# Optimization experiments

Hardware: AMD Instinct MI355X
Metric: run time of the kernel (lower is better)

Reference implementation:

```python
import jax, jax.numpy as jnp
import numpy as np

B, N, H, T = 128, 512, 128, 4

def setup_inputs() -> dict:
    key = jax.random.key(0)
    ks = jax.random.split(key, 16)
    stdv = 1.0 / np.sqrt(H)
    u = lambda k, shape: jax.random.uniform(k, shape, jnp.float32, -stdv, stdv)
    return {
        "A": jax.random.uniform(ks[0], (B, N, N), jnp.float32),
        "hidden": jax.random.normal(ks[1], (B, N, H), jnp.float32),
        "b_ah": u(ks[2], (H,)),
        "w_z": u(ks[3], (H, H)), "b_wz": u(ks[4], (H,)),
        "u_z": u(ks[5], (H, H)), "b_uz": u(ks[6], (H,)),
        "w_r": u(ks[7], (H, H)), "b_wr": u(ks[8], (H,)),
        "u_r": u(ks[9], (H, H)), "b_ur": u(ks[10], (H,)),
        "w": u(ks[11], (H, H)), "b_w": u(ks[12], (H,)),
        "u": u(ks[13], (H, H)), "b_u": u(ks[14], (H,)),
    }

def reference(A, hidden, b_ah, w_z, b_wz, u_z, b_uz, w_r, b_wr, u_r, b_ur, w, b_w, u, b_u):
    # A: [B,N,N], hidden: [B,N,H]. F.linear(x, W, b) == x @ W.T + b
    def cell(h, _):
        # a = A^T @ h + b_ah  -> [B,N,H]
        a = jnp.einsum('bmn,bmh->bnh', A, h) + b_ah
        z = jax.nn.sigmoid(a @ w_z.T + b_wz + h @ u_z.T + b_uz)
        r = jax.nn.sigmoid(a @ w_r.T + b_wr + h @ u_r.T + b_ur)
        c = jnp.tanh(a @ w.T + b_w + (r * h) @ u.T + b_u)
        h_t = (1.0 - z) * h + z * c
        return h_t, None
    h_out, _ = jax.lax.scan(cell, hidden, None, length=T)
    return h_out
```

## Files before the change

kernel.cpp:

```cpp
#include <hip/hip_runtime.h>
#include <hip/hip_fp16.h>

#define BB 128
#define NN 512
#define HH 128
#define TT 4

typedef _Float16 f16;
typedef _Float16 half8 __attribute__((ext_vector_type(8)));
typedef float floatx4 __attribute__((ext_vector_type(4)));

__device__ __forceinline__ void split1(float x, f16& hi, f16& lo) {
  hi = (f16)x;
  lo = (f16)(x - (float)hi);
}


__global__ void k_wsplit(const float* __restrict__ wz, const float* __restrict__ uz,
                         const float* __restrict__ wr, const float* __restrict__ ur,
                         const float* __restrict__ wc, const float* __restrict__ uc,
                         f16* __restrict__ whi, f16* __restrict__ wlo) {
  int mat = blockIdx.x >> 6;
  int idx = ((blockIdx.x & 63) << 8) + threadIdx.x;
  const float* src = mat==0?wz : mat==1?uz : mat==2?wr : mat==3?ur : mat==4?wc : uc;
  float v = src[idx] * 16.0f;
  f16 hi, lo; split1(v, hi, lo);
  whi[mat*16384 + idx] = hi;
  wlo[mat*16384 + idx] = lo;
}

__global__ void k_bsum(const float* __restrict__ bwz, const float* __restrict__ buz,
                       const float* __restrict__ bwr, const float* __restrict__ bur,
                       const float* __restrict__ bw,  const float* __restrict__ bu,
                       float* __restrict__ bias3) {
  int b = blockIdx.x, j = threadIdx.x;
  bias3[b*HH + j] = b==0 ? bwz[j]+buz[j] : (b==1 ? bwr[j]+bur[j] : bw[j]+bu[j]);
}

__global__ void k_copy_h0(const float* __restrict__ hin, float* __restrict__ h) {
  int v = blockIdx.x * 256 + threadIdx.x;
  ((float4*)h)[v] = ((const float4*)hin)[v];
}


__global__ __launch_bounds__(256) void k_biggemm(const float* __restrict__ A,
                                                 const float* __restrict__ h,
                                                 const float* __restrict__ b_ah,
                                                 float* __restrict__ a32) {
  __shared__ __align__(16) f16 Ah[128*64], Al[128*64], Hh[128*64], Hl[128*64];
  const int b = blockIdx.y, n0 = blockIdx.x * 128, tid = threadIdx.x;
  const int w = tid >> 6, L = tid & 63, quad = L >> 4, l16 = L & 15;
  const int rowsel = tid >> 5, colsel = tid & 31;
  const float* Ab = A + (size_t)b * NN * NN;
  const float* hb = h + (size_t)b * NN * HH;
  const floatx4 zero = {0.f, 0.f, 0.f, 0.f};
  floatx4 acc[2][8];
  for (int sr = 0; sr < 2; sr++) for (int sc = 0; sc < 8; sc++) acc[sr][sc] = zero;

  for (int mc = 0; mc < NN; mc += 64) {
    float4 va[8], vh[8];
#pragma unroll
    for (int i = 0; i < 8; i++) {
      int mm = rowsel * 8 + i;
      va[i] = *(const float4*)(Ab + (size_t)(mc + mm) * NN + n0 + colsel * 4);
      vh[i] = *(const float4*)(hb + (size_t)(mc + mm) * HH + colsel * 4);
    }
#pragma unroll
    for (int q = 0; q < 4; q++) {
      int c = colsel * 4 + q;
      half8 avh, avl, hvh, hvl;
#pragma unroll
      for (int i = 0; i < 8; i++) {
        f16 hi, lo;
        split1(((const float*)&va[i])[q], hi, lo); avh[i] = hi; avl[i] = lo;
        split1(((const float*)&vh[i])[q], hi, lo); hvh[i] = hi; hvl[i] = lo;
      }
      int blk = (rowsel ^ (c & 7)) * 8;
      *(half8*)&Ah[c*64 + blk] = avh;  *(half8*)&Al[c*64 + blk] = avl;
      *(half8*)&Hh[c*64 + blk] = hvh;  *(half8*)&Hl[c*64 + blk] = hvl;
    }
    __syncthreads();
#pragma unroll
    for (int ks = 0; ks < 2; ks++) {
      const int kb = ks * 4 + quad;
      half8 afh[2], afl[2], bfh[8], bfl[8];
      for (int sr = 0; sr < 2; sr++) {
        int c = w*32 + sr*16 + l16, o = c*64 + ((kb ^ (c & 7)) * 8);
        afh[sr] = *(const half8*)&Ah[o];
        afl[sr] = *(const half8*)&Al[o];
      }
      for (int sc = 0; sc < 8; sc++) {
        int c = sc*16 + l16, o = c*64 + ((kb ^ (c & 7)) * 8);
        bfh[sc] = *(const half8*)&Hh[o];
        bfl[sc] = *(const half8*)&Hl[o];
      }
      for (int sr = 0; sr < 2; sr++)
        for (int sc = 0; sc < 8; sc++) {
          acc[sr][sc] = __builtin_amdgcn_mfma_f32_16x16x32_f16(afh[sr], bfh[sc], acc[sr][sc], 0, 0, 0);
          acc[sr][sc] = __builtin_amdgcn_mfma_f32_16x16x32_f16(afh[sr], bfl[sc], acc[sr][sc], 0, 0, 0);
          acc[sr][sc] = __builtin_amdgcn_mfma_f32_16x16x32_f16(afl[sr], bfh[sc], acc[sr][sc], 0, 0, 0);
        }
    }
    __syncthreads();
  }
  float bah[8];
  for (int sc = 0; sc < 8; sc++) bah[sc] = b_ah[sc*16 + l16];
  float* ab = a32 + (size_t)b * NN * HH;
#pragma unroll
  for (int sr = 0; sr < 2; sr++)
    for (int rg = 0; rg < 4; rg++) {
      const int row = n0 + w*32 + sr*16 + quad*4 + rg;
      for (int sc = 0; sc < 8; sc++)
        ab[(size_t)row*HH + sc*16 + l16] = acc[sr][sc][rg] + bah[sc];
    }
}

__global__ __launch_bounds__(256) void k_gates(const float* __restrict__ a32,
                                               float* __restrict__ h,
                                               const f16* __restrict__ whi,
                                               const f16* __restrict__ wlo,
                                               const float* __restrict__ bias3) {
  __shared__ __align__(16) f16 rhh[128*136], rhl[128*136];
  const int row0 = blockIdx.x << 7, tid = threadIdx.x;
  const int w = tid >> 6, L = tid & 63, quad = L >> 4, l16 = L & 15;
  const float* ap[2]; const float* hp[2];
  for (int sr = 0; sr < 2; sr++) {
    int r = row0 + w*32 + sr*16 + l16;
    ap[sr] = a32 + (size_t)r * HH;
    hp[sr] = h + (size_t)r * HH;
  }
  half8 afh[2][4], afl[2][4];
#pragma unroll
  for (int sr = 0; sr < 2; sr++)
#pragma unroll
    for (int ks = 0; ks < 4; ks++) {
      const int ko = ks*32 + quad*8;
      float4 p = *(const float4*)(ap[sr] + ko);
      float4 q2 = *(const float4*)(ap[sr] + ko + 4);
      const float* v = (const float*)&p;
      const float* v2 = (const float*)&q2;
      for (int i = 0; i < 4; i++) { f16 hi, lo; split1(v[i],  hi, lo); afh[sr][ks][i]   = hi; afl[sr][ks][i]   = lo; }
      for (int i = 0; i < 4; i++) { f16 hi, lo; split1(v2[i], hi, lo); afh[sr][ks][i+4] = hi; afl[sr][ks][i+4] = lo; }
    }
  const floatx4 zero = {0.f, 0.f, 0.f, 0.f};
  const f16* Wz_h = whi;            const f16* Wz_l = wlo;
  const f16* Uz_h = whi + 16384;    const f16* Uz_l = wlo + 16384;
  const f16* Wr_h = whi + 2*16384;  const f16* Wr_l = wlo + 2*16384;
  const f16* Ur_h = whi + 3*16384;  const f16* Ur_l = wlo + 3*16384;
  const f16* Wc_h = whi + 4*16384;  const f16* Wc_l = wlo + 4*16384;
  const f16* Uc_h = whi + 5*16384;  const f16* Uc_l = wlo + 5*16384;

  floatx4 racc[2][8];
  for (int sr = 0; sr < 2; sr++) for (int sc = 0; sc < 8; sc++) racc[sr][sc] = zero;
#pragma unroll
  for (int ks = 0; ks < 4; ks++) {
    const int ko = ks*32 + quad*8;
    half8 hfh[2], hfl[2];
    for (int sr = 0; sr < 2; sr++) {
      float4 p = *(const float4*)(hp[sr] + ko);
      float4 q2 = *(const float4*)(hp[sr] + ko + 4);
      const float* v = (const float*)&p; const float* v2 = (const float*)&q2;
      for (int i = 0; i < 4; i++) { f16 hi, lo; split1(v[i],  hi, lo); hfh[sr][i]   = hi; hfl[sr][i]   = lo; }
      for (int i = 0; i < 4; i++) { f16 hi, lo; split1(v2[i], hi, lo); hfh[sr][i+4] = hi; hfl[sr][i+4] = lo; }
    }
#pragma unroll
    for (int sc = 0; sc < 8; sc++) {
      const int wo = (sc*16 + l16)*HH + ko;
      half8 wh = *(const half8*)(Wr_h + wo), wl = *(const half8*)(Wr_l + wo);
      half8 uh = *(const half8*)(Ur_h + wo), ul = *(const half8*)(Ur_l + wo);
      for (int sr = 0; sr < 2; sr++) {
        racc[sr][sc] = __builtin_amdgcn_mfma_f32_16x16x32_f16(afh[sr][ks], wh, racc[sr][sc], 0, 0, 0);
        racc[sr][sc] = __builtin_amdgcn_mfma_f32_16x16x32_f16(afh[sr][ks], wl, racc[sr][sc], 0, 0, 0);
        racc[sr][sc] = __builtin_amdgcn_mfma_f32_16x16x32_f16(afl[sr][ks], wh, racc[sr][sc], 0, 0, 0);
        racc[sr][sc] = __builtin_amdgcn_mfma_f32_16x16x32_f16(hfh[sr], uh, racc[sr][sc], 0, 0, 0);
        racc[sr][sc] = __builtin_amdgcn_mfma_f32_16x16x32_f16(hfh[sr], ul, racc[sr][sc], 0, 0, 0);
        racc[sr][sc] = __builtin_amdgcn_mfma_f32_16x16x32_f16(hfl[sr], uh, racc[sr][sc], 0, 0, 0);
      }
    }
  }
  {
    float brv[8];
    for (int sc = 0; sc < 8; sc++) brv[sc] = bias3[128 + sc*16 + l16];
#pragma unroll
    for (int sr = 0; sr < 2; sr++)
#pragma unroll
      for (int rg = 0; rg < 4; rg++) {
        const int lrow = w*32 + sr*16 + quad*4 + rg;
        const float* hrow = h + (size_t)(row0 + lrow)*HH;
        for (int sc = 0; sc < 8; sc++) {
          const int col = sc*16 + l16;
          float pr = racc[sr][sc][rg] * 0.0625f + brv[sc];
          float rv = 1.f / (1.f + expf(-pr));
          float rhv = rv * hrow[col];
          f16 hi, lo; split1(rhv, hi, lo);
          rhh[lrow*136 + col] = hi;
          rhl[lrow*136 + col] = lo;
        }
      }
  }
  __syncthreads();
  floatx4 cacc[2][8];
  for (int sr = 0; sr < 2; sr++) for (int sc = 0; sc < 8; sc++) cacc[sr][sc] = zero;
#pragma unroll
  for (int ks = 0; ks < 4; ks++) {
    const int ko = ks*32 + quad*8;
    half8 rfh[2], rfl[2];
    for (int sr = 0; sr < 2; sr++) {
      int o = (w*32 + sr*16 + l16)*136 + ko;
      rfh[sr] = *(const half8*)&rhh[o];
      rfl[sr] = *(const half8*)&rhl[o];
    }
#pragma unroll
    for (int sc = 0; sc < 8; sc++) {
      const int wo = (sc*16 + l16)*HH + ko;
      half8 wh = *(const half8*)(Wc_h + wo), wl = *(const half8*)(Wc_l + wo);
      half8 uh = *(const half8*)(Uc_h + wo), ul = *(const half8*)(Uc_l + wo);
      for (int sr = 0; sr < 2; sr++) {
        cacc[sr][sc] = __builtin_amdgcn_mfma_f32_16x16x32_f16(afh[sr][ks], wh, cacc[sr][sc], 0, 0, 0);
        cacc[sr][sc] = __builtin_amdgcn_mfma_f32_16x16x32_f16(afh[sr][ks], wl, cacc[sr][sc], 0, 0, 0);
        cacc[sr][sc] = __builtin_amdgcn_mfma_f32_16x16x32_f16(afl[sr][ks], wh, cacc[sr][sc], 0, 0, 0);
        cacc[sr][sc] = __builtin_amdgcn_mfma_f32_16x16x32_f16(rfh[sr], uh, cacc[sr][sc], 0, 0, 0);
        cacc[sr][sc] = __builtin_amdgcn_mfma_f32_16x16x32_f16(rfh[sr], ul, cacc[sr][sc], 0, 0, 0);
        cacc[sr][sc] = __builtin_amdgcn_mfma_f32_16x16x32_f16(rfl[sr], uh, cacc[sr][sc], 0, 0, 0);
      }
    }
  }
  floatx4 zacc[2][8];
  for (int sr = 0; sr < 2; sr++) for (int sc = 0; sc < 8; sc++) zacc[sr][sc] = zero;
#pragma unroll
  for (int ks = 0; ks < 4; ks++) {
    const int ko = ks*32 + quad*8;
    half8 hfh[2], hfl[2];
    for (int sr = 0; sr < 2; sr++) {
      float4 p = *(const float4*)(hp[sr] + ko);
      float4 q2 = *(const float4*)(hp[sr] + ko + 4);
      const float* v = (const float*)&p; const float* v2 = (const float*)&q2;
      for (int i = 0; i < 4; i++) { f16 hi, lo; split1(v[i],  hi, lo); hfh[sr][i]   = hi; hfl[sr][i]   = lo; }
      for (int i = 0; i < 4; i++) { f16 hi, lo; split1(v2[i], hi, lo); hfh[sr][i+4] = hi; hfl[sr][i+4] = lo; }
    }
#pragma unroll
    for (int sc = 0; sc < 8; sc++) {
      const int wo = (sc*16 + l16)*HH + ko;
      half8 wh = *(const half8*)(Wz_h + wo), wl = *(const half8*)(Wz_l + wo);
      half8 uh = *(const half8*)(Uz_h + wo), ul = *(const half8*)(Uz_l + wo);
      for (int sr = 0; sr < 2; sr++) {
        zacc[sr][sc] = __builtin_amdgcn_mfma_f32_16x16x32_f16(afh[sr][ks], wh, zacc[sr][sc], 0, 0, 0);
        zacc[sr][sc] = __builtin_amdgcn_mfma_f32_16x16x32_f16(afh[sr][ks], wl, zacc[sr][sc], 0, 0, 0);
        zacc[sr][sc] = __builtin_amdgcn_mfma_f32_16x16x32_f16(afl[sr][ks], wh, zacc[sr][sc], 0, 0, 0);
        zacc[sr][sc] = __builtin_amdgcn_mfma_f32_16x16x32_f16(hfh[sr], uh, zacc[sr][sc], 0, 0, 0);
        zacc[sr][sc] = __builtin_amdgcn_mfma_f32_16x16x32_f16(hfh[sr], ul, zacc[sr][sc], 0, 0, 0);
        zacc[sr][sc] = __builtin_amdgcn_mfma_f32_16x16x32_f16(hfl[sr], uh, zacc[sr][sc], 0, 0, 0);
      }
    }
  }
  float bzv[8], bcv[8];
  for (int sc = 0; sc < 8; sc++) {
    bzv[sc] = bias3[sc*16 + l16];
    bcv[sc] = bias3[256 + sc*16 + l16];
  }
#pragma unroll
  for (int sr = 0; sr < 2; sr++)
#pragma unroll
    for (int rg = 0; rg < 4; rg++) {
      const int lrow = w*32 + sr*16 + quad*4 + rg;
      float* hrow = h + (size_t)(row0 + lrow)*HH;
      for (int sc = 0; sc < 8; sc++) {
        const int col = sc*16 + l16;
        float pz = zacc[sr][sc][rg] * 0.0625f + bzv[sc];
        float zv = 1.f / (1.f + expf(-pz));
        float cv = tanhf(cacc[sr][sc][rg] * 0.0625f + bcv[sc]);
        float hv = hrow[col];
        hrow[col] = hv + zv*(cv - hv);
      }
    }
}

extern "C" void kernel_launch(void* const* d_in, const int* in_sizes, int n_in,
                              void* d_out, int out_size, void* d_ws, size_t ws_size,
                              hipStream_t stream) {
  const float* A      = (const float*)d_in[0];
  const float* hidden = (const float*)d_in[1];
  const float* b_ah   = (const float*)d_in[2];
  const float* w_z = (const float*)d_in[3];  const float* b_wz = (const float*)d_in[4];
  const float* u_z = (const float*)d_in[5];  const float* b_uz = (const float*)d_in[6];
  const float* w_r = (const float*)d_in[7];  const float* b_wr = (const float*)d_in[8];
  const float* u_r = (const float*)d_in[9];  const float* b_ur = (const float*)d_in[10];
  const float* w   = (const float*)d_in[11]; const float* b_w  = (const float*)d_in[12];
  const float* u   = (const float*)d_in[13]; const float* b_u  = (const float*)d_in[14];

  float* h = (float*)d_out;
  char* ws = (char*)d_ws;
  float* a32  = (float*)ws;
  f16*   whi  = (f16*)(ws + 33554432);
  f16*   wlo  = (f16*)(ws + 33751040);
  float* bias3= (float*)(ws + 33947648);

  k_wsplit<<<384, 256, 0, stream>>>(w_z, u_z, w_r, u_r, w, u, whi, wlo);
  k_bsum<<<3, HH, 0, stream>>>(b_wz, b_uz, b_wr, b_ur, b_w, b_u, bias3);
  k_copy_h0<<<8192, 256, 0, stream>>>(hidden, h);

  for (int t = 0; t < TT; t++) {
    k_biggemm<<<dim3(4, BB), 256, 0, stream>>>(A, h, b_ah, a32);
    k_gates<<<512, 256, 0, stream>>>(a32, h, whi, wlo, bias3);
  }
}
```

Before: 1.008 ms.

## Stage gate weights through LDS with global_load_lds and swizzled layouts

The gate kernel now copies each weight K-slice (hi and lo halves) into a small LDS buffer using global_load_lds direct-to-LDS loads, with an XOR swizzle, instead of having every wave load the weights from global memory into registers. The hidden-state hi/lo splits are computed once up front rather than recomputed per gate, the z-gate GEMM is moved ahead of the c-gate, and the r*h scratch buffer uses a swizzled layout in place of padding. Launch bounds now request two blocks per CU. In exchange it adds many __syncthreads and full vmcnt waits per K step with no double buffering, and keeping hfh/hfl live across the kernel increases register pressure.

```diff
diff --git a/kernel.cpp b/kernel.cpp
--- a/kernel.cpp
+++ b/kernel.cpp
@@ -14,6 +14,10 @@
   hi = (f16)x;
   lo = (f16)(x - (float)hi);
 }
+
+#define GLL16(gp, lp) __builtin_amdgcn_global_load_lds( \
+    (const __attribute__((address_space(1))) void*)(const void*)(gp), \
+    (__attribute__((address_space(3))) void*)(void*)(lp), 16, 0, 0)
 
 
 __global__ void k_wsplit(const float* __restrict__ wz, const float* __restrict__ uz,
@@ -115,21 +119,23 @@
     }
 }
 
-__global__ __launch_bounds__(256) void k_gates(const float* __restrict__ a32,
-                                               float* __restrict__ h,
-                                               const f16* __restrict__ whi,
-                                               const f16* __restrict__ wlo,
-                                               const float* __restrict__ bias3) {
-  __shared__ __align__(16) f16 rhh[128*136], rhl[128*136];
+__global__ __launch_bounds__(256, 2) void k_gates(const float* __restrict__ a32,
+                                                  float* __restrict__ h,
+                                                  const f16* __restrict__ whi,
+                                                  const f16* __restrict__ wlo,
+                                                  const float* __restrict__ bias3) {
+  __shared__ __align__(16) f16 wbuf[8192];
+  __shared__ __align__(16) f16 rhh[16384], rhl[16384];
   const int row0 = blockIdx.x << 7, tid = threadIdx.x;
   const int w = tid >> 6, L = tid & 63, quad = L >> 4, l16 = L & 15;
+
   const float* ap[2]; const float* hp[2];
   for (int sr = 0; sr < 2; sr++) {
     int r = row0 + w*32 + sr*16 + l16;
     ap[sr] = a32 + (size_t)r * HH;
     hp[sr] = h + (size_t)r * HH;
   }
-  half8 afh[2][4], afl[2][4];
+  half8 afh[2][4], afl[2][4], hfh[2][4], hfl[2][4];
 #pragma unroll
   for (int sr = 0; sr < 2; sr++)
 #pragma unroll
@@ -141,8 +147,32 @@
       const float* v2 = (const float*)&q2;
       for (int i = 0; i < 4; i++) { f16 hi, lo; split1(v[i],  hi, lo); afh[sr][ks][i]   = hi; afl[sr][ks][i]   = lo; }
       for (int i = 0; i < 4; i++) { f16 hi, lo; split1(v2[i], hi, lo); afh[sr][ks][i+4] = hi; afl[sr][ks][i+4] = lo; }
+      float4 hpv = *(const float4*)(hp[sr] + ko);
+      float4 hqv = *(const float4*)(hp[sr] + ko + 4);
+      const float* hv1 = (const float*)&hpv;
+      const float* hv2 = (const float*)&hqv;
+      for (int i = 0; i < 4; i++) { f16 hi, lo; split1(hv1[i], hi, lo); hfh[sr][ks][i]   = hi; hfl[sr][ks][i]   = lo; }
+      for (int i = 0; i < 4; i++) { f16 hi, lo; split1(hv2[i], hi, lo); hfh[sr][ks][i+4] = hi; hfl[sr][ks][i+4] = lo; }
     }
   const floatx4 zero = {0.f, 0.f, 0.f, 0.f};
+
+  const int rq = L >> 2;
+  const int qf = (L & 3) ^ ((L >> 3) & 3);
+  auto STAGE2 = [&](const f16* m0, const f16* m1, int ks) {
+#pragma unroll
+    for (int hf2 = 0; hf2 < 2; hf2++) {
+      const int r = hf2*64 + w*16 + rq;
+      const int go = r*HH + ks*32 + qf*8;
+      f16* lp = (f16*)wbuf + hf2*2048 + w*512;
+      GLL16(m0 + go, lp);
+      GLL16(m1 + go, lp + 4096);
+    }
+  };
+  auto LDW = [&](int mat, int sc) -> half8 {
+    const int e = mat*4096 + (sc*16 + l16)*32 + ((quad ^ ((l16>>1)&3)))*8;
+    return *(const half8*)&wbuf[e];
+  };
+
   const f16* Wz_h = whi;            const f16* Wz_l = wlo;
   const f16* Uz_h = whi + 16384;    const f16* Uz_l = wlo + 16384;
   const f16* Wr_h = whi + 2*16384;  const f16* Wr_l = wlo + 2*16384;
@@ -152,127 +182,151 @@
 
   floatx4 racc[2][8];
   for (int sr = 0; sr < 2; sr++) for (int sc = 0; sc < 8; sc++) racc[sr][sc] = zero;
-#pragma unroll
+#pragma unroll 1
   for (int ks = 0; ks < 4; ks++) {
-    const int ko = ks*32 + quad*8;
-    half8 hfh[2], hfl[2];
-    for (int sr = 0; sr < 2; sr++) {
-      float4 p = *(const float4*)(hp[sr] + ko);
-      float4 q2 = *(const float4*)(hp[sr] + ko + 4);
-      const float* v = (const float*)&p; const float* v2 = (const float*)&q2;
-      for (int i = 0; i < 4; i++) { f16 hi, lo; split1(v[i],  hi, lo); hfh[sr][i]   = hi; hfl[sr][i]   = lo; }
-      for (int i = 0; i < 4; i++) { f16 hi, lo; split1(v2[i], hi, lo); hfh[sr][i+4] = hi; hfl[sr][i+4] = lo; }
-    }
-#pragma unroll
-    for (int sc = 0; sc < 8; sc++) {
-      const int wo = (sc*16 + l16)*HH + ko;
-      half8 wh = *(const half8*)(Wr_h + wo), wl = *(const half8*)(Wr_l + wo);
-      half8 uh = *(const half8*)(Ur_h + wo), ul = *(const half8*)(Ur_l + wo);
+    STAGE2(Wr_h, Ur_h, ks);
+    asm volatile("s_waitcnt vmcnt(0)" ::: "memory");
+    __syncthreads();
+#pragma unroll
+    for (int sc = 0; sc < 8; sc++) {
+      half8 wh = LDW(0, sc), uh = LDW(1, sc);
+#pragma unroll
       for (int sr = 0; sr < 2; sr++) {
         racc[sr][sc] = __builtin_amdgcn_mfma_f32_16x16x32_f16(afh[sr][ks], wh, racc[sr][sc], 0, 0, 0);
+        racc[sr][sc] = __builtin_amdgcn_mfma_f32_16x16x32_f16(afl[sr][ks], wh, racc[sr][sc], 0, 0, 0);
+        racc[sr][sc] = __builtin_amdgcn_mfma_f32_16x16x32_f16(hfh[sr][ks], uh, racc[sr][sc], 0, 0, 0);
+        racc[sr][sc] = __builtin_amdgcn_mfma_f32_16x16x32_f16(hfl[sr][ks], uh, racc[sr][sc], 0, 0, 0);
+      }
+    }
+    __syncthreads();
+    STAGE2(Wr_l, Ur_l, ks);
+    asm volatile("s_waitcnt vmcnt(0)" ::: "memory");
+    __syncthreads();
+#pragma unroll
+    for (int sc = 0; sc < 8; sc++) {
+      half8 wl = LDW(0, sc), ul = LDW(1, sc);
+#pragma unroll
+      for (int sr = 0; sr < 2; sr++) {
         racc[sr][sc] = __builtin_amdgcn_mfma_f32_16x16x32_f16(afh[sr][ks], wl, racc[sr][sc], 0, 0, 0);
-        racc[sr][sc] = __builtin_amdgcn_mfma_f32_16x16x32_f16(afl[sr][ks], wh, racc[sr][sc], 0, 0, 0);
-        racc[sr][sc] = __builtin_amdgcn_mfma_f32_16x16x32_f16(hfh[sr], uh, racc[sr][sc], 0, 0, 0);
-        racc[sr][sc] = __builtin_amdgcn_mfma_f32_16x16x32_f16(hfh[sr], ul, racc[sr][sc], 0, 0, 0);
-        racc[sr][sc] = __builtin_amdgcn_mfma_f32_16x16x32_f16(hfl[sr], uh, racc[sr][sc], 0, 0, 0);
-      }
-    }
-  }
-  {
-    float brv[8];
-    for (int sc = 0; sc < 8; sc++) brv[sc] = bias3[128 + sc*16 + l16];
+        racc[sr][sc] = __builtin_amdgcn_mfma_f32_16x16x32_f16(hfh[sr][ks], ul, racc[sr][sc], 0, 0, 0);
+      }
+    }
+    __syncthreads();
+  }
+#pragma unroll
+  for (int sc = 0; sc < 8; sc++) {
+    const int col = sc*16 + l16;
+    const float brv = bias3[128 + col];
 #pragma unroll
     for (int sr = 0; sr < 2; sr++)
 #pragma unroll
       for (int rg = 0; rg < 4; rg++) {
         const int lrow = w*32 + sr*16 + quad*4 + rg;
         const float* hrow = h + (size_t)(row0 + lrow)*HH;
-        for (int sc = 0; sc < 8; sc++) {
-          const int col = sc*16 + l16;
-          float pr = racc[sr][sc][rg] * 0.0625f + brv[sc];
-          float rv = 1.f / (1.f + expf(-pr));
-          float rhv = rv * hrow[col];
-          f16 hi, lo; split1(rhv, hi, lo);
-          rhh[lrow*136 + col] = hi;
-          rhl[lrow*136 + col] = lo;
-        }
-      }
-  }
-  __syncthreads();
+        float pr = racc[sr][sc][rg] * 0.0625f + brv;
+        float rv = 1.f / (1.f + expf(-pr));
+        float rhv = rv * hrow[col];
+        f16 hi, lo; split1(rhv, hi, lo);
+        const int off = lrow*128 + (((col>>3) ^ (lrow&7))<<3) + (col&7);
+        rhh[off] = hi;
+        rhl[off] = lo;
+      }
+  }
+  asm volatile("s_waitcnt lgkmcnt(0)" ::: "memory");
+
+  floatx4 zacc[2][8];
+  for (int sr = 0; sr < 2; sr++) for (int sc = 0; sc < 8; sc++) zacc[sr][sc] = zero;
+#pragma unroll 1
+  for (int ks = 0; ks < 4; ks++) {
+    STAGE2(Wz_h, Uz_h, ks);
+    asm volatile("s_waitcnt vmcnt(0)" ::: "memory");
+    __syncthreads();
+#pragma unroll
+    for (int sc = 0; sc < 8; sc++) {
+      half8 wh = LDW(0, sc), uh = LDW(1, sc);
+#pragma unroll
+      for (int sr = 0; sr < 2; sr++) {
+        zacc[sr][sc] = __builtin_amdgcn_mfma_f32_16x16x32_f16(afh[sr][ks], wh, zacc[sr][sc], 0, 0, 0);
+        zacc[sr][sc] = __builtin_amdgcn_mfma_f32_16x16x32_f16(afl[sr][ks], wh, zacc[sr][sc], 0, 0, 0);
+        zacc[sr][sc] = __builtin_amdgcn_mfma_f32_16x16x32_f16(hfh[sr][ks], uh, zacc[sr][sc], 0, 0, 0);
+        zacc[sr][sc] = __builtin_amdgcn_mfma_f32_16x16x32_f16(hfl[sr][ks], uh, zacc[sr][sc], 0, 0, 0);
+      }
+    }
+    __syncthreads();
+    STAGE2(Wz_l, Uz_l, ks);
+    asm volatile("s_waitcnt vmcnt(0)" ::: "memory");
+    __syncthreads();
+#pragma unroll
+    for (int sc = 0; sc < 8; sc++) {
+      half8 wl = LDW(0, sc), ul = LDW(1, sc);
+#pragma unroll
+      for (int sr = 0; sr < 2; sr++) {
+        zacc[sr][sc] = __builtin_amdgcn_mfma_f32_16x16x32_f16(afh[sr][ks], wl, zacc[sr][sc], 0, 0, 0);
+        zacc[sr][sc] = __builtin_amdgcn_mfma_f32_16x16x32_f16(hfh[sr][ks], ul, zacc[sr][sc], 0, 0, 0);
+      }
+    }
+    __syncthreads();
+  }
+
   floatx4 cacc[2][8];
   for (int sr = 0; sr < 2; sr++) for (int sc = 0; sc < 8; sc++) cacc[sr][sc] = zero;
-#pragma unroll
+#pragma unroll 1
   for (int ks = 0; ks < 4; ks++) {
-    const int ko = ks*32 + quad*8;
     half8 rfh[2], rfl[2];
+#pragma unroll
     for (int sr = 0; sr < 2; sr++) {
-      int o = (w*32 + sr*16 + l16)*136 + ko;
-      rfh[sr] = *(const half8*)&rhh[o];
-      rfl[sr] = *(const half8*)&rhl[o];
-    }
-#pragma unroll
-    for (int sc = 0; sc < 8; sc++) {
-      const int wo = (sc*16 + l16)*HH + ko;
-      half8 wh = *(const half8*)(Wc_h + wo), wl = *(const half8*)(Wc_l + wo);
-      half8 uh = *(const half8*)(Uc_h + wo), ul = *(const half8*)(Uc_l + wo);
+      const int row = w*32 + sr*16 + l16;
+      const int off = row*128 + (((ks*4 + quad) ^ (l16 & 7)) << 3);
+      rfh[sr] = *(const half8*)&rhh[off];
+      rfl[sr] = *(const half8*)&rhl[off];
+    }
+    STAGE2(Wc_h, Uc_h, ks);
+    asm volatile("s_waitcnt vmcnt(0)" ::: "memory");
+    __syncthreads();
+#pragma unroll
+    for (int sc = 0; sc < 8; sc++) {
+      half8 wh = LDW(0, sc), uh = LDW(1, sc);
+#pragma unroll
       for (int sr = 0; sr < 2; sr++) {
         cacc[sr][sc] = __builtin_amdgcn_mfma_f32_16x16x32_f16(afh[sr][ks], wh, cacc[sr][sc], 0, 0, 0);
-        cacc[sr][sc] = __builtin_amdgcn_mfma_f32_16x16x32_f16(afh[sr][ks], wl, cacc[sr][sc], 0, 0, 0);
         cacc[sr][sc] = __builtin_amdgcn_mfma_f32_16x16x32_f16(afl[sr][ks], wh, cacc[sr][sc], 0, 0, 0);
         cacc[sr][sc] = __builtin_amdgcn_mfma_f32_16x16x32_f16(rfh[sr], uh, cacc[sr][sc], 0, 0, 0);
+        cacc[sr][sc] = __builtin_amdgcn_mfma_f32_16x16x32_f16(rfl[sr], uh, cacc[sr][sc], 0, 0, 0);
+      }
+    }
+    __syncthreads();
+    STAGE2(Wc_l, Uc_l, ks);
+    asm volatile("s_waitcnt vmcnt(0)" ::: "memory");
+    __syncthreads();
+#pragma unroll
+    for (int sc = 0; sc < 8; sc++) {
+      half8 wl = LDW(0, sc), ul = LDW(1, sc);
+#pragma unroll
+      for (int sr = 0; sr < 2; sr++) {
+        cacc[sr][sc] = __builtin_amdgcn_mfma_f32_16x16x32_f16(afh[sr][ks], wl, cacc[sr][sc], 0, 0, 0);
         cacc[sr][sc] = __builtin_amdgcn_mfma_f32_16x16x32_f16(rfh[sr], ul, cacc[sr][sc], 0, 0, 0);
-        cacc[sr][sc] = __builtin_amdgcn_mfma_f32_16x16x32_f16(rfl[sr], uh, cacc[sr][sc], 0, 0, 0);
-      }
-    }
-  }
-  floatx4 zacc[2][8];
-  for (int sr = 0; sr < 2; sr++) for (int sc = 0; sc < 8; sc++) zacc[sr][sc] = zero;
-#pragma unroll
-  for (int ks = 0; ks < 4; ks++) {
-    const int ko = ks*32 + quad*8;
-    half8 hfh[2], hfl[2];
-    for (int sr = 0; sr < 2; sr++) {
-      float4 p = *(const float4*)(hp[sr] + ko);
-      float4 q2 = *(const float4*)(hp[sr] + ko + 4);
-      const float* v = (const float*)&p; const float* v2 = (const float*)&q2;
-      for (int i = 0; i < 4; i++) { f16 hi, lo; split1(v[i],  hi, lo); hfh[sr][i]   = hi; hfl[sr][i]   = lo; }
-      for (int i = 0; i < 4; i++) { f16 hi, lo; split1(v2[i], hi, lo); hfh[sr][i+4] = hi; hfl[sr][i+4] = lo; }
-    }
-#pragma unroll
-    for (int sc = 0; sc < 8; sc++) {
-      const int wo = (sc*16 + l16)*HH + ko;
-      half8 wh = *(const half8*)(Wz_h + wo), wl = *(const half8*)(Wz_l + wo);
-      half8 uh = *(const half8*)(Uz_h + wo), ul = *(const half8*)(Uz_l + wo);
-      for (int sr = 0; sr < 2; sr++) {
-        zacc[sr][sc] = __builtin_amdgcn_mfma_f32_16x16x32_f16(afh[sr][ks], wh, zacc[sr][sc], 0, 0, 0);
-        zacc[sr][sc] = __builtin_amdgcn_mfma_f32_16x16x32_f16(afh[sr][ks], wl, zacc[sr][sc], 0, 0, 0);
-        zacc[sr][sc] = __builtin_amdgcn_mfma_f32_16x16x32_f16(afl[sr][ks], wh, zacc[sr][sc], 0, 0, 0);
-        zacc[sr][sc] = __builtin_amdgcn_mfma_f32_16x16x32_f16(hfh[sr], uh, zacc[sr][sc], 0, 0, 0);
-        zacc[sr][sc] = __builtin_amdgcn_mfma_f32_16x16x32_f16(hfh[sr], ul, zacc[sr][sc], 0, 0, 0);
-        zacc[sr][sc] = __builtin_amdgcn_mfma_f32_16x16x32_f16(hfl[sr], uh, zacc[sr][sc], 0, 0, 0);
-      }
-    }
-  }
-  float bzv[8], bcv[8];
+      }
+    }
+    __syncthreads();
+  }
+#pragma unroll
   for (int sc = 0; sc < 8; sc++) {
-    bzv[sc] = bias3[sc*16 + l16];
-    bcv[sc] = bias3[256 + sc*16 + l16];
-  }
-#pragma unroll
-  for (int sr = 0; sr < 2; sr++)
-#pragma unroll
-    for (int rg = 0; rg < 4; rg++) {
-      const int lrow = w*32 + sr*16 + quad*4 + rg;
-      float* hrow = h + (size_t)(row0 + lrow)*HH;
-      for (int sc = 0; sc < 8; sc++) {
-        const int col = sc*16 + l16;
-        float pz = zacc[sr][sc][rg] * 0.0625f + bzv[sc];
+    const int col = sc*16 + l16;
+    const float bzv = bias3[col];
+    const float bcv = bias3[256 + col];
+#pragma unroll
+    for (int sr = 0; sr < 2; sr++)
+#pragma unroll
+      for (int rg = 0; rg < 4; rg++) {
+        const int lrow = w*32 + sr*16 + quad*4 + rg;
+        float* hrow = h + (size_t)(row0 + lrow)*HH;
+        float pz = zacc[sr][sc][rg] * 0.0625f + bzv;
         float zv = 1.f / (1.f + expf(-pz));
-        float cv = tanhf(cacc[sr][sc][rg] * 0.0625f + bcv[sc]);
+        float cv = tanhf(cacc[sr][sc][rg] * 0.0625f + bcv);
         float hv = hrow[col];
         hrow[col] = hv + zv*(cv - hv);
       }
-    }
+  }
 }
 
 extern "C" void kernel_launch(void* const* d_in, const int* in_sizes, int n_in,
```

After: 2.873 ms. +184.9%, slower.
